# Kernel optimization log

Measured on AMD Instinct MI355X. Metric: run time of the kernel, lower is better.

Reference implementation:

```python
import jax, jax.numpy as jnp
import numpy as np

D_MODEL = 1024
NUM_HEADS = 16
D_FF = 4096
EPS = 1e-5


def _linear(x, w, b):
    # torch nn.Linear: y = x @ W^T + b, W is [out, in]
    return jnp.einsum('bld,od->blo', x, w) + b


def _layer_norm(x, g, b):
    mu = jnp.mean(x, axis=-1, keepdims=True)
    var = jnp.mean(jnp.square(x - mu), axis=-1, keepdims=True)
    return (x - mu) / jnp.sqrt(var + EPS) * g + b


def _mha(q, k, v, wq, bq, wk, bk, wv, bv, wo, bo, mask, num_heads):
    B, Lq, D = q.shape
    hd = D // num_heads
    Q = _linear(q, wq, bq).reshape(B, Lq, num_heads, hd).transpose(0, 2, 1, 3)
    K = _linear(k, wk, bk).reshape(B, -1, num_heads, hd).transpose(0, 2, 1, 3)
    V = _linear(v, wv, bv).reshape(B, -1, num_heads, hd).transpose(0, 2, 1, 3)
    scale = jnp.sqrt(jnp.asarray(hd, dtype=q.dtype))
    energy = jnp.einsum('bhqd,bhkd->bhqk', Q, K) / scale  # [B,H,Lq,Lk]
    energy = jnp.where(mask, energy, jnp.asarray(-1e10, dtype=q.dtype))
    attn = jax.nn.softmax(energy, axis=-1)
    x = jnp.einsum('bhqk,bhkd->bhqd', attn, V)
    x = x.transpose(0, 2, 1, 3).reshape(B, Lq, D)
    return _linear(x, wo, bo), attn


def setup_inputs() -> dict:
    key = jax.random.key(0)
    ks = iter(jax.random.split(key, 40))
    B, T, S, D, F = 4, 1024, 1024, D_MODEL, D_FF
    inp = {
        'tgt': jax.random.normal(next(ks), (B, T, D), dtype=jnp.float32),
        'enc_src': jax.random.normal(next(ks), (B, S, D), dtype=jnp.float32),
        'tgt_mask': jnp.tril(jnp.ones((1, 1, T, T), dtype=bool)),
        'src_mask': jnp.ones((1, 1, 1, S), dtype=bool),
    }
    def lin(kk, o, i):
        return jax.random.normal(kk, (o, i), dtype=jnp.float32) * 0.02
    for pfx in ('sa', 'ca'):  # self-attn and cross-attn params
        for nm in ('q', 'k', 'v', 'o'):
            inp[f'{pfx}_w{nm}'] = lin(next(ks), D, D)
            inp[f'{pfx}_b{nm}'] = jnp.zeros((D,), dtype=jnp.float32)
    inp['ff_w1'] = lin(next(ks), F, D)
    inp['ff_b1'] = jnp.zeros((F,), dtype=jnp.float32)
    inp['ff_w2'] = lin(next(ks), D, F)
    inp['ff_b2'] = jnp.zeros((D,), dtype=jnp.float32)
    for i in (1, 2, 3):
        inp[f'ln{i}_g'] = jnp.ones((D,), dtype=jnp.float32)
        inp[f'ln{i}_b'] = jnp.zeros((D,), dtype=jnp.float32)
    return inp


def reference(tgt, enc_src, tgt_mask, src_mask,
              sa_wq, sa_bq, sa_wk, sa_bk, sa_wv, sa_bv, sa_wo, sa_bo,
              ca_wq, ca_bq, ca_wk, ca_bk, ca_wv, ca_bv, ca_wo, ca_bo,
              ff_w1, ff_b1, ff_w2, ff_b2,
              ln1_g, ln1_b, ln2_g, ln2_b, ln3_g, ln3_b):
    # dropout in eval mode (identity)
    _t, _ = _mha(tgt, tgt, tgt, sa_wq, sa_bq, sa_wk, sa_bk, sa_wv, sa_bv,
                 sa_wo, sa_bo, tgt_mask, NUM_HEADS)
    tgt = _layer_norm(tgt + _t, ln1_g, ln1_b)
    _t, attention = _mha(tgt, enc_src, enc_src, ca_wq, ca_bq, ca_wk, ca_bk,
                         ca_wv, ca_bv, ca_wo, ca_bo, src_mask, NUM_HEADS)
    tgt = _layer_norm(tgt + _t, ln2_g, ln2_b)
    _t = _linear(jax.nn.relu(_linear(tgt, ff_w1, ff_b1)), ff_w2, ff_b2)
    tgt = _layer_norm(tgt + _t, ln3_g, ln3_b)
    return tgt, attention
```

## Files before the change

kernel.cpp:

```cpp
#include <hip/hip_runtime.h>
#include <hip/hip_bf16.h>

#define BBATCH 4
#define TT 1024
#define SS 1024
#define DD 1024
#define HH 16
#define HD 64
#define FFD 4096
#define MM (BBATCH*TT)

using f32x4  = __attribute__((ext_vector_type(4))) float;
using s16x8  = __attribute__((ext_vector_type(8))) short;
using bf16x8 = __attribute__((ext_vector_type(8))) __bf16;

__device__ __forceinline__ unsigned short f2b(float f) {
  union { float f; unsigned int u; } x{f};
  unsigned int r = x.u + 0x7FFFu + ((x.u >> 16) & 1u);
  return (unsigned short)(r >> 16);
}

__device__ __forceinline__ void gload16(const void* g, void* l) {
  __builtin_amdgcn_global_load_lds(
      (const __attribute__((address_space(1))) void*)g,
      (__attribute__((address_space(3))) void*)l, 16, 0, 0);
}

__device__ __forceinline__ f32x4 mfma_bf16(s16x8 a, s16x8 b, f32x4 c) {
  return __builtin_amdgcn_mfma_f32_16x16x32_bf16(
      __builtin_bit_cast(bf16x8, a), __builtin_bit_cast(bf16x8, b), c, 0, 0, 0);
}

template <int JT>
__device__ __forceinline__ void gemm_core(
    const unsigned short* __restrict__ Ab, int lda,
    const unsigned short* __restrict__ Bb, int ldb,
    int K, unsigned short* As, unsigned short* Bs, f32x4 (&acc)[4][JT])
{
  const int tid = threadIdx.x, wave = tid >> 6, lane = tid & 63;
  const int r0 = tid >> 2, c0 = (tid & 3) * 8;
  const int wrow = (wave >> 1) * 64, wcol = (wave & 1) * 16 * JT;
  const int q = lane >> 4, rl = lane & 15;
  const s16x8* Av = (const s16x8*)As;
  const s16x8* Bv = (const s16x8*)Bs;

  for (int k0 = 0; k0 < K; k0 += 32) {
    gload16(Ab + (size_t)r0 * lda + k0 + c0, As + wave * 512);
    gload16(Ab + (size_t)(r0 + 64) * lda + k0 + c0, As + wave * 512 + 2048);
    gload16(Bb + (size_t)r0 * ldb + k0 + c0, Bs + wave * 512);
    if (JT == 4)
      gload16(Bb + (size_t)(r0 + 64) * ldb + k0 + c0, Bs + wave * 512 + 2048);
    __syncthreads();
    s16x8 af[4], bfr[JT];
#pragma unroll
    for (int t = 0; t < 4; t++) af[t] = Av[(wrow + t * 16 + rl) * 4 + q];
#pragma unroll
    for (int t = 0; t < JT; t++) bfr[t] = Bv[(wcol + t * 16 + rl) * 4 + q];
#pragma unroll
    for (int i = 0; i < 4; i++)
#pragma unroll
      for (int j = 0; j < JT; j++)
        acc[i][j] = mfma_bf16(af[i], bfr[j], acc[i][j]);
    __syncthreads();
  }
}

template <int EPI, int JT>
__global__ __launch_bounds__(256) void gemm_bt(
    const unsigned short* __restrict__ A, int lda,
    const unsigned short* __restrict__ B, int ldb,
    const float* __restrict__ bias, const float* __restrict__ res,
    float* __restrict__ Cf, unsigned short* __restrict__ Cb, int ldc, int K)
{
  __shared__ __align__(16) unsigned short As[128 * 32];
  __shared__ __align__(16) unsigned short Bs[JT * 1024];
  const int bm = blockIdx.y, bn = blockIdx.x;
  const int lane = threadIdx.x & 63, wave = threadIdx.x >> 6;
  const int wrow = (wave >> 1) * 64, wcol = (wave & 1) * 16 * JT;
  const int q = lane >> 4, rl = lane & 15;

  f32x4 acc[4][JT];
  f32x4 z = {0.f, 0.f, 0.f, 0.f};
#pragma unroll
  for (int i = 0; i < 4; i++)
#pragma unroll
    for (int j = 0; j < JT; j++) acc[i][j] = z;

  gemm_core<JT>(A + (size_t)bm * 128 * lda, lda,
                B + (size_t)bn * (32 * JT) * ldb, ldb, K, As, Bs, acc);

#pragma unroll
  for (int i = 0; i < 4; i++) {
    int gm0 = bm * 128 + wrow + i * 16 + q * 4;
#pragma unroll
    for (int j = 0; j < JT; j++) {
      int gn = bn * (32 * JT) + wcol + j * 16 + rl;
      float bv = bias[gn];
#pragma unroll
      for (int r = 0; r < 4; r++) {
        size_t off = (size_t)(gm0 + r) * ldc + gn;
        float v = acc[i][j][r];
        if constexpr (EPI == 0) Cb[off] = f2b(v + bv);
        else if constexpr (EPI == 2) Cf[off] = v + bv + res[off];
        else Cb[off] = f2b(fmaxf(v + bv, 0.f));
      }
    }
  }
}

__device__ __forceinline__ void sblock_qk(
    const unsigned short* Qs, const unsigned short* Ks,
    int wrow, int wcol, int q, int rl, f32x4 (&acc)[4][4])
{
  const s16x8* Qv = (const s16x8*)Qs;
  const s16x8* Kv = (const s16x8*)Ks;
  f32x4 z = {0.f, 0.f, 0.f, 0.f};
#pragma unroll
  for (int i = 0; i < 4; i++)
#pragma unroll
    for (int j = 0; j < 4; j++) acc[i][j] = z;
#pragma unroll
  for (int kq = 0; kq < 2; kq++) {
    s16x8 af[4], bf[4];
#pragma unroll
    for (int t = 0; t < 4; t++) af[t] = Qv[kq * 512 + (wrow + t * 16 + rl) * 4 + q];
#pragma unroll
    for (int t = 0; t < 4; t++) bf[t] = Kv[kq * 512 + (wcol + t * 16 + rl) * 4 + q];
#pragma unroll
    for (int i = 0; i < 4; i++)
#pragma unroll
      for (int j = 0; j < 4; j++)
        acc[i][j] = mfma_bf16(af[i], bf[j], acc[i][j]);
  }
}

__global__ __launch_bounds__(256, 2) void flash_sa(
    const unsigned short* __restrict__ Qg, int ldq,
    const unsigned short* __restrict__ Kg, int ldk,
    const unsigned short* __restrict__ Vt,
    unsigned short* __restrict__ Og)
{
  __shared__ __align__(16) unsigned short Qs[2 * 128 * 32];
  __shared__ __align__(16) unsigned short KP[4 * 128 * 40];
  __shared__ __align__(16) unsigned short Vs[4 * 64 * 32];
  __shared__ float red[2][128];

  const int tid = threadIdx.x, wave = tid >> 6, lane = tid & 63;
  const int q = lane >> 4, rl = lane & 15;
  const int bm = blockIdx.x, bh = blockIdx.y, b = bh >> 4, h = bh & 15;
  const int wrow = (wave >> 1) * 64, wcol = (wave & 1) * 64;
  const int wc2 = (wave & 1) * 32;
  const int r0 = tid >> 2, c0 = (tid & 3) * 8;

  const unsigned short* Qbase = Qg + ((size_t)b * TT + bm * 128) * ldq + h * HD;
  const unsigned short* Kbase = Kg + (size_t)b * SS * ldk + h * HD;
  const unsigned short* Vbase = Vt + ((size_t)bh << 16);

#pragma unroll
  for (int kq = 0; kq < 2; kq++) {
    gload16(Qbase + (size_t)r0 * ldq + kq * 32 + c0, Qs + kq * 4096 + wave * 512);
    gload16(Qbase + (size_t)(r0 + 64) * ldq + kq * 32 + c0, Qs + kq * 4096 + wave * 512 + 2048);
  }
  const int nch = bm + 1;
  const float NEG = -3.0e38f;

  float m_run[4][4], l_run[4][4];
  f32x4 oacc[4][2];
  f32x4 z = {0.f, 0.f, 0.f, 0.f};
#pragma unroll
  for (int i = 0; i < 4; i++) {
    oacc[i][0] = z; oacc[i][1] = z;
#pragma unroll
    for (int r = 0; r < 4; r++) { m_run[i][r] = NEG; l_run[i][r] = 0.f; }
  }

  for (int c = 0; c < nch; c++) {
    const unsigned short* src = Kbase + (size_t)c * 128 * ldk;
#pragma unroll
    for (int kq = 0; kq < 2; kq++) {
      gload16(src + (size_t)r0 * ldk + kq * 32 + c0, KP + kq * 4096 + wave * 512);
      gload16(src + (size_t)(r0 + 64) * ldk + kq * 32 + c0, KP + kq * 4096 + wave * 512 + 2048);
    }
#pragma unroll
    for (int ks = 0; ks < 4; ks++)
      gload16(Vbase + (size_t)r0 * SS + c * 128 + ks * 32 + c0, Vs + ks * 2048 + wave * 512);
    __syncthreads();

    f32x4 acc[4][4];
    sblock_qk(Qs, KP, wrow, wcol, q, rl, acc);
#pragma unroll
    for (int i = 0; i < 4; i++)
#pragma unroll
      for (int j = 0; j < 4; j++)
#pragma unroll
        for (int r = 0; r < 4; r++) {
          float v = acc[i][j][r] * 0.125f;
          if (c == bm && (wcol + j * 16 + rl) > (wrow + i * 16 + q * 4 + r)) v = NEG;
          acc[i][j][r] = v;
        }
    float mx[4][4];
#pragma unroll
    for (int i = 0; i < 4; i++)
#pragma unroll
      for (int r = 0; r < 4; r++) {
        float m0 = fmaxf(fmaxf(acc[i][0][r], acc[i][1][r]), fmaxf(acc[i][2][r], acc[i][3][r]));
#pragma unroll
        for (int off = 1; off < 16; off <<= 1) m0 = fmaxf(m0, __shfl_xor(m0, off));
        mx[i][r] = m0;
      }
    if (rl == 0) {
#pragma unroll
      for (int i = 0; i < 4; i++)
#pragma unroll
        for (int r = 0; r < 4; r++)
          red[wave & 1][wrow + i * 16 + q * 4 + r] = mx[i][r];
    }
    __syncthreads();
    float mn[4][4];
#pragma unroll
    for (int i = 0; i < 4; i++)
#pragma unroll
      for (int r = 0; r < 4; r++) {
        int row = wrow + i * 16 + q * 4 + r;
        mn[i][r] = fmaxf(m_run[i][r], fmaxf(red[0][row], red[1][row]));
      }
    float cs[4][4];
#pragma unroll
    for (int i = 0; i < 4; i++)
#pragma unroll
      for (int r = 0; r < 4; r++) {
#pragma unroll
        for (int j = 0; j < 4; j++) acc[i][j][r] = __expf(acc[i][j][r] - mn[i][r]);
        float s = acc[i][0][r] + acc[i][1][r] + acc[i][2][r] + acc[i][3][r];
#pragma unroll
        for (int off = 1; off < 16; off <<= 1) s += __shfl_xor(s, off);
        cs[i][r] = s;
      }
    __syncthreads();
    if (rl == 0) {
#pragma unroll
      for (int i = 0; i < 4; i++)
#pragma unroll
        for (int r = 0; r < 4; r++)
          red[wave & 1][wrow + i * 16 + q * 4 + r] = cs[i][r];
    }
    __syncthreads();
#pragma unroll
    for (int i = 0; i < 4; i++)
#pragma unroll
      for (int r = 0; r < 4; r++) {
        int row = wrow + i * 16 + q * 4 + r;
        float tot = red[0][row] + red[1][row];
        float al = __expf(m_run[i][r] - mn[i][r]);
        l_run[i][r] = l_run[i][r] * al + tot;
        m_run[i][r] = mn[i][r];
        oacc[i][0][r] *= al;
        oacc[i][1][r] *= al;
      }
#pragma unroll
    for (int i = 0; i < 4; i++)
#pragma unroll
      for (int j = 0; j < 4; j++) {
        int col = wcol + j * 16 + rl;
        int ks = col >> 5, cc = col & 31;
#pragma unroll
        for (int r = 0; r < 4; r++)
          KP[ks * 5120 + (wrow + i * 16 + q * 4 + r) * 40 + cc] = f2b(acc[i][j][r]);
      }
    __syncthreads();
    const s16x8* Pv = (const s16x8*)KP;
    const s16x8* Vv = (const s16x8*)Vs;
#pragma unroll
    for (int ks = 0; ks < 4; ks++) {
      s16x8 af[4], bf[2];
#pragma unroll
      for (int t = 0; t < 4; t++) af[t] = Pv[ks * 640 + (wrow + t * 16 + rl) * 5 + q];
#pragma unroll
      for (int t = 0; t < 2; t++) bf[t] = Vv[ks * 256 + (wc2 + t * 16 + rl) * 4 + q];
#pragma unroll
      for (int i = 0; i < 4; i++)
#pragma unroll
        for (int jt = 0; jt < 2; jt++)
          oacc[i][jt] = mfma_bf16(af[i], bf[jt], oacc[i][jt]);
    }
    __syncthreads();
  }

  float invl[4][4];
#pragma unroll
  for (int i = 0; i < 4; i++)
#pragma unroll
    for (int r = 0; r < 4; r++) invl[i][r] = 1.0f / l_run[i][r];

#pragma unroll
  for (int i = 0; i < 4; i++)
#pragma unroll
    for (int jt = 0; jt < 2; jt++)
#pragma unroll
      for (int r = 0; r < 4; r++) {
        int row = bm * 128 + wrow + i * 16 + q * 4 + r;
        int col = h * HD + wc2 + jt * 16 + rl;
        Og[((size_t)b * TT + row) * DD + col] = f2b(oacc[i][jt][r] * invl[i][r]);
      }
}

template <bool CAUSAL, bool WRITE_P>
__global__ __launch_bounds__(256, 2) void flash_attn(
    const unsigned short* __restrict__ Qg, int ldq,
    const unsigned short* __restrict__ Kg, int ldk,
    const unsigned short* __restrict__ Vt,
    float* __restrict__ Pout,
    unsigned short* __restrict__ Og)
{
  __shared__ __align__(16) unsigned short Qs[2 * 128 * 32];
  __shared__ __align__(16) unsigned short KP[4 * 128 * 40];
  __shared__ __align__(16) unsigned short Vs[4 * 64 * 32];
  __shared__ float red[2][128];

  const int tid = threadIdx.x, wave = tid >> 6, lane = tid & 63;
  const int q = lane >> 4, rl = lane & 15;
  const int bm = blockIdx.x, bh = blockIdx.y, b = bh >> 4, h = bh & 15;
  const int wrow = (wave >> 1) * 64, wcol = (wave & 1) * 64;
  const int r0 = tid >> 2, c0 = (tid & 3) * 8;

  const unsigned short* Qbase = Qg + ((size_t)b * TT + bm * 128) * ldq + h * HD;
  const unsigned short* Kbase = Kg + (size_t)b * SS * ldk + h * HD;
  const unsigned short* Vbase = Vt + ((size_t)bh << 16);

#pragma unroll
  for (int kq = 0; kq < 2; kq++) {
    gload16(Qbase + (size_t)r0 * ldq + kq * 32 + c0, Qs + kq * 4096 + wave * 512);
    gload16(Qbase + (size_t)(r0 + 64) * ldq + kq * 32 + c0, Qs + kq * 4096 + wave * 512 + 2048);
  }
  const int nch = CAUSAL ? bm + 1 : 8;
  const float NEG = -3.0e38f;

  float m_run[4][4], l_run[4][4];
#pragma unroll
  for (int i = 0; i < 4; i++)
#pragma unroll
    for (int r = 0; r < 4; r++) { m_run[i][r] = NEG; l_run[i][r] = 0.f; }

  for (int c = 0; c < nch; c++) {
    const unsigned short* src = Kbase + (size_t)c * 128 * ldk;
#pragma unroll
    for (int kq = 0; kq < 2; kq++) {
      gload16(src + (size_t)r0 * ldk + kq * 32 + c0, KP + kq * 4096 + wave * 512);
      gload16(src + (size_t)(r0 + 64) * ldk + kq * 32 + c0, KP + kq * 4096 + wave * 512 + 2048);
    }
    __syncthreads();
    f32x4 acc[4][4];
    sblock_qk(Qs, KP, wrow, wcol, q, rl, acc);
#pragma unroll
    for (int i = 0; i < 4; i++)
#pragma unroll
      for (int j = 0; j < 4; j++)
#pragma unroll
        for (int r = 0; r < 4; r++) {
          float v = acc[i][j][r] * 0.125f;
          if (CAUSAL && c == bm && (wcol + j * 16 + rl) > (wrow + i * 16 + q * 4 + r)) v = NEG;
          acc[i][j][r] = v;
        }
    float mx[4][4];
#pragma unroll
    for (int i = 0; i < 4; i++)
#pragma unroll
      for (int r = 0; r < 4; r++) {
        float m0 = fmaxf(fmaxf(acc[i][0][r], acc[i][1][r]), fmaxf(acc[i][2][r], acc[i][3][r]));
#pragma unroll
        for (int off = 1; off < 16; off <<= 1) m0 = fmaxf(m0, __shfl_xor(m0, off));
        mx[i][r] = m0;
      }
    if (rl == 0) {
#pragma unroll
      for (int i = 0; i < 4; i++)
#pragma unroll
        for (int r = 0; r < 4; r++)
          red[wave & 1][wrow + i * 16 + q * 4 + r] = mx[i][r];
    }
    __syncthreads();
    float mn[4][4];
#pragma unroll
    for (int i = 0; i < 4; i++)
#pragma unroll
      for (int r = 0; r < 4; r++) {
        int row = wrow + i * 16 + q * 4 + r;
        mn[i][r] = fmaxf(m_run[i][r], fmaxf(red[0][row], red[1][row]));
      }
    float cs[4][4];
#pragma unroll
    for (int i = 0; i < 4; i++)
#pragma unroll
      for (int r = 0; r < 4; r++) {
        float s = __expf(acc[i][0][r] - mn[i][r]) + __expf(acc[i][1][r] - mn[i][r]) +
                  __expf(acc[i][2][r] - mn[i][r]) + __expf(acc[i][3][r] - mn[i][r]);
#pragma unroll
        for (int off = 1; off < 16; off <<= 1) s += __shfl_xor(s, off);
        cs[i][r] = s;
      }
    __syncthreads();
    if (rl == 0) {
#pragma unroll
      for (int i = 0; i < 4; i++)
#pragma unroll
        for (int r = 0; r < 4; r++)
          red[wave & 1][wrow + i * 16 + q * 4 + r] = cs[i][r];
    }
    __syncthreads();
#pragma unroll
    for (int i = 0; i < 4; i++)
#pragma unroll
      for (int r = 0; r < 4; r++) {
        int row = wrow + i * 16 + q * 4 + r;
        float tot = red[0][row] + red[1][row];
        l_run[i][r] = l_run[i][r] * __expf(m_run[i][r] - mn[i][r]) + tot;
        m_run[i][r] = mn[i][r];
      }
    __syncthreads();
  }

  float invl[4][4];
#pragma unroll
  for (int i = 0; i < 4; i++)
#pragma unroll
    for (int r = 0; r < 4; r++) invl[i][r] = 1.0f / l_run[i][r];

  const int wc2 = (wave & 1) * 32;
  f32x4 oacc[4][2];
  f32x4 z = {0.f, 0.f, 0.f, 0.f};
#pragma unroll
  for (int i = 0; i < 4; i++) { oacc[i][0] = z; oacc[i][1] = z; }

  for (int c = 0; c < nch; c++) {
    __syncthreads();
    const unsigned short* src = Kbase + (size_t)c * 128 * ldk;
#pragma unroll
    for (int kq = 0; kq < 2; kq++) {
      gload16(src + (size_t)r0 * ldk + kq * 32 + c0, KP + kq * 4096 + wave * 512);
      gload16(src + (size_t)(r0 + 64) * ldk + kq * 32 + c0, KP + kq * 4096 + wave * 512 + 2048);
    }
#pragma unroll
    for (int ks = 0; ks < 4; ks++)
      gload16(Vbase + (size_t)r0 * SS + c * 128 + ks * 32 + c0, Vs + ks * 2048 + wave * 512);
    __syncthreads();
    f32x4 acc[4][4];
    sblock_qk(Qs, KP, wrow, wcol, q, rl, acc);
#pragma unroll
    for (int i = 0; i < 4; i++)
#pragma unroll
      for (int j = 0; j < 4; j++)
#pragma unroll
        for (int r = 0; r < 4; r++) {
          float v = acc[i][j][r] * 0.125f;
          bool msk = CAUSAL && c == bm && (wcol + j * 16 + rl) > (wrow + i * 16 + q * 4 + r);
          acc[i][j][r] = msk ? 0.f : __expf(v - m_run[i][r]) * invl[i][r];
        }
    if (WRITE_P) {
      float* Pb = Pout + ((size_t)bh << 20) +
                  ((size_t)(bm * 128 + wrow + q * 4) << 10) + c * 128 + wcol + rl;
#pragma unroll
      for (int i = 0; i < 4; i++)
#pragma unroll
        for (int r = 0; r < 4; r++)
#pragma unroll
          for (int j = 0; j < 4; j++)
            Pb[(size_t)((i * 16 + r) << 10) + j * 16] = acc[i][j][r];
    }
    __syncthreads();
#pragma unroll
    for (int i = 0; i < 4; i++)
#pragma unroll
      for (int j = 0; j < 4; j++) {
        int col = wcol + j * 16 + rl;
        int ks = col >> 5, cc = col & 31;
#pragma unroll
        for (int r = 0; r < 4; r++)
          KP[ks * 5120 + (wrow + i * 16 + q * 4 + r) * 40 + cc] = f2b(acc[i][j][r]);
      }
    __syncthreads();
    const s16x8* Pv = (const s16x8*)KP;
    const s16x8* Vv = (const s16x8*)Vs;
#pragma unroll
    for (int ks = 0; ks < 4; ks++) {
      s16x8 af[4], bf[2];
#pragma unroll
      for (int t = 0; t < 4; t++) af[t] = Pv[ks * 640 + (wrow + t * 16 + rl) * 5 + q];
#pragma unroll
      for (int t = 0; t < 2; t++) bf[t] = Vv[ks * 256 + (wc2 + t * 16 + rl) * 4 + q];
#pragma unroll
      for (int i = 0; i < 4; i++)
#pragma unroll
        for (int jt = 0; jt < 2; jt++)
          oacc[i][jt] = mfma_bf16(af[i], bf[jt], oacc[i][jt]);
    }
  }

#pragma unroll
  for (int i = 0; i < 4; i++)
#pragma unroll
    for (int jt = 0; jt < 2; jt++)
#pragma unroll
      for (int r = 0; r < 4; r++) {
        int row = bm * 128 + wrow + i * 16 + q * 4 + r;
        int col = h * HD + wc2 + jt * 16 + rl;
        Og[((size_t)b * TT + row) * DD + col] = f2b(oacc[i][jt][r]);
      }
}

__global__ __launch_bounds__(256) void transpose_v(
    const unsigned short* __restrict__ V, int ldv, unsigned short* __restrict__ Vt)
{
  __shared__ unsigned short tile[64][68];
  const int bh = blockIdx.z, b = bh >> 4, h = bh & 15;
  const int s0 = blockIdx.x * 64;
  const int tid = threadIdx.x;
#pragma unroll
  for (int i = 0; i < 4; i++) {
    int idx = i * 256 + tid;
    int sl = idx >> 4, d0 = (idx & 15) * 4;
    ushort4 v = *(const ushort4*)&V[((size_t)b * SS + s0 + sl) * ldv + h * HD + d0];
    tile[sl][d0] = v.x; tile[sl][d0 + 1] = v.y; tile[sl][d0 + 2] = v.z; tile[sl][d0 + 3] = v.w;
  }
  __syncthreads();
#pragma unroll
  for (int i = 0; i < 4; i++) {
    int idx = i * 256 + tid;
    int d = idx >> 4, s4 = (idx & 15) * 4;
    ushort4 o = make_ushort4(tile[s4][d], tile[s4 + 1][d], tile[s4 + 2][d], tile[s4 + 3][d]);
    *(ushort4*)&Vt[((size_t)bh * HD + d) * SS + s0 + s4] = o;
  }
}

__global__ __launch_bounds__(256) void ln_k(
    const float* __restrict__ src, const float* __restrict__ g,
    const float* __restrict__ b, float* __restrict__ dstf,
    unsigned short* __restrict__ dstb)
{
  __shared__ float sh[10];
  const size_t row = blockIdx.x;
  const int tid = threadIdx.x;
  float4 v = ((const float4*)(src + (row << 10)))[tid];
  float s = v.x + v.y + v.z + v.w;
  float ss = v.x * v.x + v.y * v.y + v.z * v.z + v.w * v.w;
  for (int o = 32; o; o >>= 1) { s += __shfl_down(s, o); ss += __shfl_down(ss, o); }
  if ((tid & 63) == 0) { sh[tid >> 6] = s; sh[4 + (tid >> 6)] = ss; }
  __syncthreads();
  if (tid == 0) {
    sh[8] = sh[0] + sh[1] + sh[2] + sh[3];
    sh[9] = sh[4] + sh[5] + sh[6] + sh[7];
  }
  __syncthreads();
  const float mean = sh[8] * (1.0f / DD);
  const float var = sh[9] * (1.0f / DD) - mean * mean;
  const float inv = rsqrtf(var + 1e-5f);
  float4 gv = ((const float4*)g)[tid];
  float4 bv = ((const float4*)b)[tid];
  float4 y;
  y.x = (v.x - mean) * inv * gv.x + bv.x;
  y.y = (v.y - mean) * inv * gv.y + bv.y;
  y.z = (v.z - mean) * inv * gv.z + bv.z;
  y.w = (v.w - mean) * inv * gv.w + bv.w;
  if (dstf) ((float4*)(dstf + (row << 10)))[tid] = y;
  if (dstb) {
    ushort4 o = make_ushort4(f2b(y.x), f2b(y.y), f2b(y.z), f2b(y.w));
    ((ushort4*)(dstb + (row << 10)))[tid] = o;
  }
}

struct CvtArgs {
  const float* src[12];
  unsigned short* dst[12];
};

__global__ __launch_bounds__(256) void cvt_all(CvtArgs a) {
  constexpr int st[13] = {0,       1048576, 2097152, 2359296, 2621440,
                          2883584, 3145728, 3407872, 3670016, 3932160,
                          4194304, 5242880, 6291456};
  int i = blockIdx.x * 256 + threadIdx.x;
  int s = 0;
#pragma unroll
  for (int k = 1; k < 12; k++) s += (i >= st[k]) ? 1 : 0;
  int j = i - st[s];
  float4 v = ((const float4*)a.src[s])[j];
  ushort4 o = make_ushort4(f2b(v.x), f2b(v.y), f2b(v.z), f2b(v.w));
  ((ushort4*)a.dst[s])[j] = o;
}

__global__ __launch_bounds__(256) void bias_pack(
    const float* __restrict__ bq, const float* __restrict__ bk, const float* __restrict__ bv,
    const float* __restrict__ bk2, const float* __restrict__ bv2,
    float* __restrict__ bqkv, float* __restrict__ bkv)
{
  int i = blockIdx.x * 256 + threadIdx.x;
  if (i < 1024) bqkv[i] = bq[i];
  else if (i < 2048) bqkv[i] = bk[i - 1024];
  else if (i < 3072) bqkv[i] = bv[i - 2048];
  else if (i < 4096) bkv[i - 3072] = bk2[i - 3072];
  else if (i < 5120) bkv[i - 3072] = bv2[i - 4096 + 1024];
}


extern "C" void kernel_launch(void* const* d_in, const int* in_sizes, int n_in,
                              void* d_out, int out_size, void* d_ws, size_t ws_size,
                              hipStream_t stream)
{
  const float* tgt = (const float*)d_in[0];
  const float* enc = (const float*)d_in[1];
  const float* sa_wq = (const float*)d_in[4];  const float* sa_bq = (const float*)d_in[5];
  const float* sa_wk = (const float*)d_in[6];  const float* sa_bk = (const float*)d_in[7];
  const float* sa_wv = (const float*)d_in[8];  const float* sa_bv = (const float*)d_in[9];
  const float* sa_wo = (const float*)d_in[10]; const float* sa_bo = (const float*)d_in[11];
  const float* ca_wq = (const float*)d_in[12]; const float* ca_bq = (const float*)d_in[13];
  const float* ca_wk = (const float*)d_in[14]; const float* ca_bk = (const float*)d_in[15];
  const float* ca_wv = (const float*)d_in[16]; const float* ca_bv = (const float*)d_in[17];
  const float* ca_wo = (const float*)d_in[18]; const float* ca_bo = (const float*)d_in[19];
  const float* ff_w1 = (const float*)d_in[20]; const float* ff_b1 = (const float*)d_in[21];
  const float* ff_w2 = (const float*)d_in[22]; const float* ff_b2 = (const float*)d_in[23];
  const float* ln1_g = (const float*)d_in[24]; const float* ln1_b = (const float*)d_in[25];
  const float* ln2_g = (const float*)d_in[26]; const float* ln2_b = (const float*)d_in[27];
  const float* ln3_g = (const float*)d_in[28]; const float* ln3_b = (const float*)d_in[29];

  float* out_tgt = (float*)d_out;
  float* out_attn = (float*)d_out + (size_t)MM * DD;

  char* w = (char*)d_ws;
  size_t off = 0;
  auto alloc = [&](size_t bytes) { void* p = w + off; off += (bytes + 255) & ~(size_t)255; return p; };
  unsigned short* Xb   = (unsigned short*)alloc((size_t)MM * DD * 2);
  unsigned short* Eb   = (unsigned short*)alloc((size_t)MM * DD * 2);
  unsigned short* Wq1  = (unsigned short*)alloc((size_t)DD * DD * 2);
  unsigned short* Wk1  = (unsigned short*)alloc((size_t)DD * DD * 2);
  unsigned short* Wv1  = (unsigned short*)alloc((size_t)DD * DD * 2);
  unsigned short* Wo1  = (unsigned short*)alloc((size_t)DD * DD * 2);
  unsigned short* Wq2  = (unsigned short*)alloc((size_t)DD * DD * 2);
  unsigned short* Wk2  = (unsigned short*)alloc((size_t)DD * DD * 2);
  unsigned short* Wv2  = (unsigned short*)alloc((size_t)DD * DD * 2);
  unsigned short* Wo2  = (unsigned short*)alloc((size_t)DD * DD * 2);
  unsigned short* Wf1  = (unsigned short*)alloc((size_t)FFD * DD * 2);
  unsigned short* Wf2  = (unsigned short*)alloc((size_t)DD * FFD * 2);
  unsigned short* QKVb = (unsigned short*)alloc((size_t)MM * 3 * DD * 2);
  unsigned short* KVb  = (unsigned short*)alloc((size_t)MM * 2 * DD * 2);
  unsigned short* Qca  = (unsigned short*)alloc((size_t)MM * DD * 2);
  unsigned short* Vt   = (unsigned short*)alloc((size_t)MM * DD * 2);
  unsigned short* Ob   = (unsigned short*)alloc((size_t)MM * DD * 2);
  float*          res1 = (float*)alloc((size_t)MM * DD * 4);
  unsigned short* t1b  = (unsigned short*)alloc((size_t)MM * DD * 2);
  float*          res2 = (float*)alloc((size_t)MM * DD * 4);
  unsigned short* t2b  = (unsigned short*)alloc((size_t)MM * DD * 2);
  unsigned short* Fb   = (unsigned short*)alloc((size_t)MM * FFD * 2);
  float*          bqkv = (float*)alloc(3072 * 4);
  float*          bkv  = (float*)alloc(2048 * 4);

  CvtArgs ca;
  ca.src[0] = tgt;   ca.dst[0] = Xb;
  ca.src[1] = enc;   ca.dst[1] = Eb;
  ca.src[2] = sa_wq; ca.dst[2] = Wq1;
  ca.src[3] = sa_wk; ca.dst[3] = Wk1;
  ca.src[4] = sa_wv; ca.dst[4] = Wv1;
  ca.src[5] = sa_wo; ca.dst[5] = Wo1;
  ca.src[6] = ca_wq; ca.dst[6] = Wq2;
  ca.src[7] = ca_wk; ca.dst[7] = Wk2;
  ca.src[8] = ca_wv; ca.dst[8] = Wv2;
  ca.src[9] = ca_wo; ca.dst[9] = Wo2;
  ca.src[10] = ff_w1; ca.dst[10] = Wf1;
  ca.src[11] = ff_w2; ca.dst[11] = Wf2;

  bias_pack<<<20, 256, 0, stream>>>(sa_bq, sa_bk, sa_bv, ca_bk, ca_bv, bqkv, bkv);
  cvt_all<<<24576, 256, 0, stream>>>(ca);

  const dim3 gQKV(24, 32);
  const dim3 gKV(16, 32);
  const dim3 gN64(16, 32);
  const dim3 gFF1(32, 32);
  const dim3 gFl(8, 64);
  const dim3 gTr(SS / 64, 1, BBATCH * HH);

  gemm_bt<0, 4><<<gQKV, 256, 0, stream>>>(Xb, DD, Wq1, DD, bqkv, nullptr, nullptr, QKVb, 3 * DD, DD);
  transpose_v<<<gTr, 256, 0, stream>>>(QKVb + 2 * DD, 3 * DD, Vt);
  flash_sa<<<gFl, 256, 0, stream>>>(QKVb, 3 * DD, QKVb + DD, 3 * DD, Vt, Ob);
  gemm_bt<2, 2><<<gN64, 256, 0, stream>>>(Ob, DD, Wo1, DD, sa_bo, tgt, res1, nullptr, DD, DD);
  ln_k<<<MM, 256, 0, stream>>>(res1, ln1_g, ln1_b, res1, t1b);

  gemm_bt<0, 2><<<gN64, 256, 0, stream>>>(t1b, DD, Wq2, DD, ca_bq, nullptr, nullptr, Qca, DD, DD);
  gemm_bt<0, 4><<<gKV, 256, 0, stream>>>(Eb, DD, Wk2, DD, bkv, nullptr, nullptr, KVb, 2 * DD, DD);
  transpose_v<<<gTr, 256, 0, stream>>>(KVb + DD, 2 * DD, Vt);
  flash_attn<false, true><<<gFl, 256, 0, stream>>>(Qca, DD, KVb, 2 * DD, Vt, out_attn, Ob);
  gemm_bt<2, 2><<<gN64, 256, 0, stream>>>(Ob, DD, Wo2, DD, ca_bo, res1, res2, nullptr, DD, DD);
  ln_k<<<MM, 256, 0, stream>>>(res2, ln2_g, ln2_b, res2, t2b);

  gemm_bt<3, 4><<<gFF1, 256, 0, stream>>>(t2b, DD, Wf1, DD, ff_b1, nullptr, nullptr, Fb, FFD, DD);
  gemm_bt<2, 2><<<gN64, 256, 0, stream>>>(Fb, FFD, Wf2, FFD, ff_b2, res2, res1, nullptr, DD, FFD);
  ln_k<<<MM, 256, 0, stream>>>(res1, ln3_g, ln3_b, out_tgt, nullptr);
}
```

Baseline: 866.4 us.

## Load K/V fragments directly from global, swizzle LDS, trim syncs, widen N-tiles

The flash attention kernels now read K and V MFMA fragments straight from global memory into registers instead of staging them through LDS. Q and P use an XOR-swizzled unpadded LDS layout in place of padded rows. Separate max and sum reduction buffers let several __syncthreads calls be removed. The cross-attention kernel becomes a dedicated non-templated version, and the N=1024 GEMMs switch to 128-wide N tiles with half the grid. The trade-off is less LDS traffic and barrier cost against uncoalesced per-lane global loads for K and V and lower GEMM block counts.

```diff
diff --git a/kernel.cpp b/kernel.cpp
--- a/kernel.cpp
+++ b/kernel.cpp
@@ -108,12 +108,22 @@
   }
 }
 
-__device__ __forceinline__ void sblock_qk(
-    const unsigned short* Qs, const unsigned short* Ks,
-    int wrow, int wcol, int q, int rl, f32x4 (&acc)[4][4])
+__device__ __forceinline__ void load_kf(
+    const unsigned short* Kp, int ldk, int wcol, int q, int rl, s16x8 (&kf)[2][4])
+{
+#pragma unroll
+  for (int j = 0; j < 4; j++) {
+    const unsigned short* p = Kp + (size_t)(wcol + j * 16 + rl) * ldk + q * 8;
+    kf[0][j] = *(const s16x8*)p;
+    kf[1][j] = *(const s16x8*)(p + 32);
+  }
+}
+
+__device__ __forceinline__ void qk_swz(
+    const unsigned short* Qs, const s16x8 (&kf)[2][4],
+    int wrow, int q, int rl, f32x4 (&acc)[4][4])
 {
   const s16x8* Qv = (const s16x8*)Qs;
-  const s16x8* Kv = (const s16x8*)Ks;
   f32x4 z = {0.f, 0.f, 0.f, 0.f};
 #pragma unroll
   for (int i = 0; i < 4; i++)
@@ -121,16 +131,59 @@
     for (int j = 0; j < 4; j++) acc[i][j] = z;
 #pragma unroll
   for (int kq = 0; kq < 2; kq++) {
-    s16x8 af[4], bf[4];
-#pragma unroll
-    for (int t = 0; t < 4; t++) af[t] = Qv[kq * 512 + (wrow + t * 16 + rl) * 4 + q];
-#pragma unroll
-    for (int t = 0; t < 4; t++) bf[t] = Kv[kq * 512 + (wcol + t * 16 + rl) * 4 + q];
+    s16x8 af[4];
+#pragma unroll
+    for (int t = 0; t < 4; t++) {
+      int row = wrow + t * 16 + rl;
+      af[t] = Qv[kq * 512 + ((row * 4 + q) ^ ((row >> 1) & 3))];
+    }
 #pragma unroll
     for (int i = 0; i < 4; i++)
 #pragma unroll
       for (int j = 0; j < 4; j++)
-        acc[i][j] = mfma_bf16(af[i], bf[j], acc[i][j]);
+        acc[i][j] = mfma_bf16(af[i], kf[kq][j], acc[i][j]);
+  }
+}
+
+__device__ __forceinline__ void store_ps(
+    unsigned short* Ps, const f32x4 (&acc)[4][4],
+    int wrow, int wcol, int q, int rl)
+{
+#pragma unroll
+  for (int i = 0; i < 4; i++)
+#pragma unroll
+    for (int j = 0; j < 4; j++) {
+      int col = wcol + j * 16 + rl;
+      int ks = col >> 5, cc = col & 31;
+#pragma unroll
+      for (int r = 0; r < 4; r++) {
+        int row = wrow + i * 16 + q * 4 + r;
+        Ps[ks * 4096 + ((row * 32 + cc) ^ (((row >> 1) & 3) << 3))] = f2b(acc[i][j][r]);
+      }
+    }
+}
+
+__device__ __forceinline__ void pv_accum(
+    const unsigned short* Ps, const unsigned short* Vbase, int c,
+    int wrow, int wc2, int q, int rl, f32x4 (&oacc)[4][2])
+{
+  const s16x8* Pv = (const s16x8*)Ps;
+#pragma unroll
+  for (int ks = 0; ks < 4; ks++) {
+    s16x8 af[4], bf[2];
+#pragma unroll
+    for (int t = 0; t < 4; t++) {
+      int row = wrow + t * 16 + rl;
+      af[t] = Pv[ks * 512 + ((row * 4 + q) ^ ((row >> 1) & 3))];
+    }
+#pragma unroll
+    for (int t = 0; t < 2; t++)
+      bf[t] = *(const s16x8*)(Vbase + (size_t)(wc2 + t * 16 + rl) * SS + c * 128 + ks * 32 + q * 8);
+#pragma unroll
+    for (int i = 0; i < 4; i++)
+#pragma unroll
+      for (int jt = 0; jt < 2; jt++)
+        oacc[i][jt] = mfma_bf16(af[i], bf[jt], oacc[i][jt]);
   }
 }
 
@@ -141,16 +194,16 @@
     unsigned short* __restrict__ Og)
 {
   __shared__ __align__(16) unsigned short Qs[2 * 128 * 32];
-  __shared__ __align__(16) unsigned short KP[4 * 128 * 40];
-  __shared__ __align__(16) unsigned short Vs[4 * 64 * 32];
-  __shared__ float red[2][128];
+  __shared__ __align__(16) unsigned short Ps[4 * 128 * 32];
+  __shared__ float redm[2][128], reds[2][128];
 
   const int tid = threadIdx.x, wave = tid >> 6, lane = tid & 63;
   const int q = lane >> 4, rl = lane & 15;
   const int bm = blockIdx.x, bh = blockIdx.y, b = bh >> 4, h = bh & 15;
   const int wrow = (wave >> 1) * 64, wcol = (wave & 1) * 64;
   const int wc2 = (wave & 1) * 32;
-  const int r0 = tid >> 2, c0 = (tid & 3) * 8;
+  const int r0 = tid >> 2;
+  const int c0s = ((tid & 3) ^ ((r0 >> 1) & 3)) * 8;
 
   const unsigned short* Qbase = Qg + ((size_t)b * TT + bm * 128) * ldq + h * HD;
   const unsigned short* Kbase = Kg + (size_t)b * SS * ldk + h * HD;
@@ -158,8 +211,8 @@
 
 #pragma unroll
   for (int kq = 0; kq < 2; kq++) {
-    gload16(Qbase + (size_t)r0 * ldq + kq * 32 + c0, Qs + kq * 4096 + wave * 512);
-    gload16(Qbase + (size_t)(r0 + 64) * ldq + kq * 32 + c0, Qs + kq * 4096 + wave * 512 + 2048);
+    gload16(Qbase + (size_t)r0 * ldq + kq * 32 + c0s, Qs + kq * 4096 + wave * 512);
+    gload16(Qbase + (size_t)(r0 + 64) * ldq + kq * 32 + c0s, Qs + kq * 4096 + wave * 512 + 2048);
   }
   const int nch = bm + 1;
   const float NEG = -3.0e38f;
@@ -173,21 +226,14 @@
 #pragma unroll
     for (int r = 0; r < 4; r++) { m_run[i][r] = NEG; l_run[i][r] = 0.f; }
   }
+  __syncthreads();
 
   for (int c = 0; c < nch; c++) {
-    const unsigned short* src = Kbase + (size_t)c * 128 * ldk;
-#pragma unroll
-    for (int kq = 0; kq < 2; kq++) {
-      gload16(src + (size_t)r0 * ldk + kq * 32 + c0, KP + kq * 4096 + wave * 512);
-      gload16(src + (size_t)(r0 + 64) * ldk + kq * 32 + c0, KP + kq * 4096 + wave * 512 + 2048);
-    }
-#pragma unroll
-    for (int ks = 0; ks < 4; ks++)
-      gload16(Vbase + (size_t)r0 * SS + c * 128 + ks * 32 + c0, Vs + ks * 2048 + wave * 512);
-    __syncthreads();
-
+    const unsigned short* Kp = Kbase + (size_t)c * 128 * ldk;
+    s16x8 kf[2][4];
+    load_kf(Kp, ldk, wcol, q, rl, kf);
     f32x4 acc[4][4];
-    sblock_qk(Qs, KP, wrow, wcol, q, rl, acc);
+    qk_swz(Qs, kf, wrow, q, rl, acc);
 #pragma unroll
     for (int i = 0; i < 4; i++)
 #pragma unroll
@@ -213,22 +259,16 @@
       for (int i = 0; i < 4; i++)
 #pragma unroll
         for (int r = 0; r < 4; r++)
-          red[wave & 1][wrow + i * 16 + q * 4 + r] = mx[i][r];
-    }
-    __syncthreads();
-    float mn[4][4];
+          redm[wave & 1][wrow + i * 16 + q * 4 + r] = mx[i][r];
+    }
+    __syncthreads();
+    float mn[4][4], cs[4][4];
 #pragma unroll
     for (int i = 0; i < 4; i++)
 #pragma unroll
       for (int r = 0; r < 4; r++) {
         int row = wrow + i * 16 + q * 4 + r;
-        mn[i][r] = fmaxf(m_run[i][r], fmaxf(red[0][row], red[1][row]));
-      }
-    float cs[4][4];
-#pragma unroll
-    for (int i = 0; i < 4; i++)
-#pragma unroll
-      for (int r = 0; r < 4; r++) {
+        mn[i][r] = fmaxf(m_run[i][r], fmaxf(redm[0][row], redm[1][row]));
 #pragma unroll
         for (int j = 0; j < 4; j++) acc[i][j][r] = __expf(acc[i][j][r] - mn[i][r]);
         float s = acc[i][0][r] + acc[i][1][r] + acc[i][2][r] + acc[i][3][r];
@@ -236,13 +276,13 @@
         for (int off = 1; off < 16; off <<= 1) s += __shfl_xor(s, off);
         cs[i][r] = s;
       }
-    __syncthreads();
+    store_ps(Ps, acc, wrow, wcol, q, rl);
     if (rl == 0) {
 #pragma unroll
       for (int i = 0; i < 4; i++)
 #pragma unroll
         for (int r = 0; r < 4; r++)
-          red[wave & 1][wrow + i * 16 + q * 4 + r] = cs[i][r];
+          reds[wave & 1][wrow + i * 16 + q * 4 + r] = cs[i][r];
     }
     __syncthreads();
 #pragma unroll
@@ -250,62 +290,32 @@
 #pragma unroll
       for (int r = 0; r < 4; r++) {
         int row = wrow + i * 16 + q * 4 + r;
-        float tot = red[0][row] + red[1][row];
+        float tot = reds[0][row] + reds[1][row];
         float al = __expf(m_run[i][r] - mn[i][r]);
         l_run[i][r] = l_run[i][r] * al + tot;
         m_run[i][r] = mn[i][r];
         oacc[i][0][r] *= al;
         oacc[i][1][r] *= al;
       }
-#pragma unroll
-    for (int i = 0; i < 4; i++)
-#pragma unroll
-      for (int j = 0; j < 4; j++) {
-        int col = wcol + j * 16 + rl;
-        int ks = col >> 5, cc = col & 31;
-#pragma unroll
-        for (int r = 0; r < 4; r++)
-          KP[ks * 5120 + (wrow + i * 16 + q * 4 + r) * 40 + cc] = f2b(acc[i][j][r]);
-      }
-    __syncthreads();
-    const s16x8* Pv = (const s16x8*)KP;
-    const s16x8* Vv = (const s16x8*)Vs;
-#pragma unroll
-    for (int ks = 0; ks < 4; ks++) {
-      s16x8 af[4], bf[2];
-#pragma unroll
-      for (int t = 0; t < 4; t++) af[t] = Pv[ks * 640 + (wrow + t * 16 + rl) * 5 + q];
-#pragma unroll
-      for (int t = 0; t < 2; t++) bf[t] = Vv[ks * 256 + (wc2 + t * 16 + rl) * 4 + q];
-#pragma unroll
-      for (int i = 0; i < 4; i++)
-#pragma unroll
-        for (int jt = 0; jt < 2; jt++)
-          oacc[i][jt] = mfma_bf16(af[i], bf[jt], oacc[i][jt]);
-    }
-    __syncthreads();
-  }
-
-  float invl[4][4];
-#pragma unroll
-  for (int i = 0; i < 4; i++)
-#pragma unroll
-    for (int r = 0; r < 4; r++) invl[i][r] = 1.0f / l_run[i][r];
-
-#pragma unroll
-  for (int i = 0; i < 4; i++)
-#pragma unroll
-    for (int jt = 0; jt < 2; jt++)
-#pragma unroll
-      for (int r = 0; r < 4; r++) {
-        int row = bm * 128 + wrow + i * 16 + q * 4 + r;
+    pv_accum(Ps, Vbase, c, wrow, wc2, q, rl, oacc);
+  }
+
+#pragma unroll
+  for (int i = 0; i < 4; i++) {
+#pragma unroll
+    for (int r = 0; r < 4; r++) {
+      float inv = 1.0f / l_run[i][r];
+      int row = bm * 128 + wrow + i * 16 + q * 4 + r;
+#pragma unroll
+      for (int jt = 0; jt < 2; jt++) {
         int col = h * HD + wc2 + jt * 16 + rl;
-        Og[((size_t)b * TT + row) * DD + col] = f2b(oacc[i][jt][r] * invl[i][r]);
-      }
-}
-
-template <bool CAUSAL, bool WRITE_P>
-__global__ __launch_bounds__(256, 2) void flash_attn(
+        Og[((size_t)b * TT + row) * DD + col] = f2b(oacc[i][jt][r] * inv);
+      }
+    }
+  }
+}
+
+__global__ __launch_bounds__(256, 2) void flash_ca(
     const unsigned short* __restrict__ Qg, int ldq,
     const unsigned short* __restrict__ Kg, int ldk,
     const unsigned short* __restrict__ Vt,
@@ -313,15 +323,16 @@
     unsigned short* __restrict__ Og)
 {
   __shared__ __align__(16) unsigned short Qs[2 * 128 * 32];
-  __shared__ __align__(16) unsigned short KP[4 * 128 * 40];
-  __shared__ __align__(16) unsigned short Vs[4 * 64 * 32];
-  __shared__ float red[2][128];
+  __shared__ __align__(16) unsigned short Ps[4 * 128 * 32];
+  __shared__ float redm[2][128], reds[2][128];
 
   const int tid = threadIdx.x, wave = tid >> 6, lane = tid & 63;
   const int q = lane >> 4, rl = lane & 15;
   const int bm = blockIdx.x, bh = blockIdx.y, b = bh >> 4, h = bh & 15;
   const int wrow = (wave >> 1) * 64, wcol = (wave & 1) * 64;
-  const int r0 = tid >> 2, c0 = (tid & 3) * 8;
+  const int wc2 = (wave & 1) * 32;
+  const int r0 = tid >> 2;
+  const int c0s = ((tid & 3) ^ ((r0 >> 1) & 3)) * 8;
 
   const unsigned short* Qbase = Qg + ((size_t)b * TT + bm * 128) * ldq + h * HD;
   const unsigned short* Kbase = Kg + (size_t)b * SS * ldk + h * HD;
@@ -329,10 +340,9 @@
 
 #pragma unroll
   for (int kq = 0; kq < 2; kq++) {
-    gload16(Qbase + (size_t)r0 * ldq + kq * 32 + c0, Qs + kq * 4096 + wave * 512);
-    gload16(Qbase + (size_t)(r0 + 64) * ldq + kq * 32 + c0, Qs + kq * 4096 + wave * 512 + 2048);
-  }
-  const int nch = CAUSAL ? bm + 1 : 8;
+    gload16(Qbase + (size_t)r0 * ldq + kq * 32 + c0s, Qs + kq * 4096 + wave * 512);
+    gload16(Qbase + (size_t)(r0 + 64) * ldq + kq * 32 + c0s, Qs + kq * 4096 + wave * 512 + 2048);
+  }
   const float NEG = -3.0e38f;
 
   float m_run[4][4], l_run[4][4];
@@ -340,32 +350,20 @@
   for (int i = 0; i < 4; i++)
 #pragma unroll
     for (int r = 0; r < 4; r++) { m_run[i][r] = NEG; l_run[i][r] = 0.f; }
-
-  for (int c = 0; c < nch; c++) {
-    const unsigned short* src = Kbase + (size_t)c * 128 * ldk;
-#pragma unroll
-    for (int kq = 0; kq < 2; kq++) {
-      gload16(src + (size_t)r0 * ldk + kq * 32 + c0, KP + kq * 4096 + wave * 512);
-      gload16(src + (size_t)(r0 + 64) * ldk + kq * 32 + c0, KP + kq * 4096 + wave * 512 + 2048);
-    }
-    __syncthreads();
+  __syncthreads();
+
+  for (int c = 0; c < 8; c++) {
+    s16x8 kf[2][4];
+    load_kf(Kbase + (size_t)c * 128 * ldk, ldk, wcol, q, rl, kf);
     f32x4 acc[4][4];
-    sblock_qk(Qs, KP, wrow, wcol, q, rl, acc);
-#pragma unroll
-    for (int i = 0; i < 4; i++)
-#pragma unroll
-      for (int j = 0; j < 4; j++)
-#pragma unroll
-        for (int r = 0; r < 4; r++) {
-          float v = acc[i][j][r] * 0.125f;
-          if (CAUSAL && c == bm && (wcol + j * 16 + rl) > (wrow + i * 16 + q * 4 + r)) v = NEG;
-          acc[i][j][r] = v;
-        }
+    qk_swz(Qs, kf, wrow, q, rl, acc);
     float mx[4][4];
 #pragma unroll
     for (int i = 0; i < 4; i++)
 #pragma unroll
       for (int r = 0; r < 4; r++) {
+#pragma unroll
+        for (int j = 0; j < 4; j++) acc[i][j][r] *= 0.125f;
         float m0 = fmaxf(fmaxf(acc[i][0][r], acc[i][1][r]), fmaxf(acc[i][2][r], acc[i][3][r]));
 #pragma unroll
         for (int off = 1; off < 16; off <<= 1) m0 = fmaxf(m0, __shfl_xor(m0, off));
@@ -376,35 +374,28 @@
       for (int i = 0; i < 4; i++)
 #pragma unroll
         for (int r = 0; r < 4; r++)
-          red[wave & 1][wrow + i * 16 + q * 4 + r] = mx[i][r];
-    }
-    __syncthreads();
-    float mn[4][4];
+          redm[wave & 1][wrow + i * 16 + q * 4 + r] = mx[i][r];
+    }
+    __syncthreads();
+    float mn[4][4], cs[4][4];
 #pragma unroll
     for (int i = 0; i < 4; i++)
 #pragma unroll
       for (int r = 0; r < 4; r++) {
         int row = wrow + i * 16 + q * 4 + r;
-        mn[i][r] = fmaxf(m_run[i][r], fmaxf(red[0][row], red[1][row]));
-      }
-    float cs[4][4];
-#pragma unroll
-    for (int i = 0; i < 4; i++)
-#pragma unroll
-      for (int r = 0; r < 4; r++) {
+        mn[i][r] = fmaxf(m_run[i][r], fmaxf(redm[0][row], redm[1][row]));
         float s = __expf(acc[i][0][r] - mn[i][r]) + __expf(acc[i][1][r] - mn[i][r]) +
                   __expf(acc[i][2][r] - mn[i][r]) + __expf(acc[i][3][r] - mn[i][r]);
 #pragma unroll
         for (int off = 1; off < 16; off <<= 1) s += __shfl_xor(s, off);
         cs[i][r] = s;
       }
-    __syncthreads();
     if (rl == 0) {
 #pragma unroll
       for (int i = 0; i < 4; i++)
 #pragma unroll
         for (int r = 0; r < 4; r++)
-          red[wave & 1][wrow + i * 16 + q * 4 + r] = cs[i][r];
+          reds[wave & 1][wrow + i * 16 + q * 4 + r] = cs[i][r];
     }
     __syncthreads();
 #pragma unroll
@@ -412,11 +403,10 @@
 #pragma unroll
       for (int r = 0; r < 4; r++) {
         int row = wrow + i * 16 + q * 4 + r;
-        float tot = red[0][row] + red[1][row];
+        float tot = reds[0][row] + reds[1][row];
         l_run[i][r] = l_run[i][r] * __expf(m_run[i][r] - mn[i][r]) + tot;
         m_run[i][r] = mn[i][r];
       }
-    __syncthreads();
   }
 
   float invl[4][4];
@@ -425,74 +415,36 @@
 #pragma unroll
     for (int r = 0; r < 4; r++) invl[i][r] = 1.0f / l_run[i][r];
 
-  const int wc2 = (wave & 1) * 32;
   f32x4 oacc[4][2];
   f32x4 z = {0.f, 0.f, 0.f, 0.f};
 #pragma unroll
   for (int i = 0; i < 4; i++) { oacc[i][0] = z; oacc[i][1] = z; }
 
-  for (int c = 0; c < nch; c++) {
-    __syncthreads();
-    const unsigned short* src = Kbase + (size_t)c * 128 * ldk;
-#pragma unroll
-    for (int kq = 0; kq < 2; kq++) {
-      gload16(src + (size_t)r0 * ldk + kq * 32 + c0, KP + kq * 4096 + wave * 512);
-      gload16(src + (size_t)(r0 + 64) * ldk + kq * 32 + c0, KP + kq * 4096 + wave * 512 + 2048);
-    }
-#pragma unroll
-    for (int ks = 0; ks < 4; ks++)
-      gload16(Vbase + (size_t)r0 * SS + c * 128 + ks * 32 + c0, Vs + ks * 2048 + wave * 512);
-    __syncthreads();
+  for (int c = 0; c < 8; c++) {
+    s16x8 kf[2][4];
+    load_kf(Kbase + (size_t)c * 128 * ldk, ldk, wcol, q, rl, kf);
     f32x4 acc[4][4];
-    sblock_qk(Qs, KP, wrow, wcol, q, rl, acc);
+    qk_swz(Qs, kf, wrow, q, rl, acc);
 #pragma unroll
     for (int i = 0; i < 4; i++)
 #pragma unroll
       for (int j = 0; j < 4; j++)
 #pragma unroll
-        for (int r = 0; r < 4; r++) {
-          float v = acc[i][j][r] * 0.125f;
-          bool msk = CAUSAL && c == bm && (wcol + j * 16 + rl) > (wrow + i * 16 + q * 4 + r);
-          acc[i][j][r] = msk ? 0.f : __expf(v - m_run[i][r]) * invl[i][r];
-        }
-    if (WRITE_P) {
-      float* Pb = Pout + ((size_t)bh << 20) +
-                  ((size_t)(bm * 128 + wrow + q * 4) << 10) + c * 128 + wcol + rl;
-#pragma unroll
-      for (int i = 0; i < 4; i++)
-#pragma unroll
         for (int r = 0; r < 4; r++)
-#pragma unroll
-          for (int j = 0; j < 4; j++)
-            Pb[(size_t)((i * 16 + r) << 10) + j * 16] = acc[i][j][r];
-    }
-    __syncthreads();
-#pragma unroll
-    for (int i = 0; i < 4; i++)
-#pragma unroll
-      for (int j = 0; j < 4; j++) {
-        int col = wcol + j * 16 + rl;
-        int ks = col >> 5, cc = col & 31;
-#pragma unroll
-        for (int r = 0; r < 4; r++)
-          KP[ks * 5120 + (wrow + i * 16 + q * 4 + r) * 40 + cc] = f2b(acc[i][j][r]);
-      }
-    __syncthreads();
-    const s16x8* Pv = (const s16x8*)KP;
-    const s16x8* Vv = (const s16x8*)Vs;
-#pragma unroll
-    for (int ks = 0; ks < 4; ks++) {
-      s16x8 af[4], bf[2];
-#pragma unroll
-      for (int t = 0; t < 4; t++) af[t] = Pv[ks * 640 + (wrow + t * 16 + rl) * 5 + q];
-#pragma unroll
-      for (int t = 0; t < 2; t++) bf[t] = Vv[ks * 256 + (wc2 + t * 16 + rl) * 4 + q];
-#pragma unroll
-      for (int i = 0; i < 4; i++)
-#pragma unroll
-        for (int jt = 0; jt < 2; jt++)
-          oacc[i][jt] = mfma_bf16(af[i], bf[jt], oacc[i][jt]);
-    }
+          acc[i][j][r] = __expf(acc[i][j][r] * 0.125f - m_run[i][r]) * invl[i][r];
+    float* Pb = Pout + ((size_t)bh << 20) +
+                ((size_t)(bm * 128 + wrow + q * 4) << 10) + c * 128 + wcol + rl;
+#pragma unroll
+    for (int i = 0; i < 4; i++)
+#pragma unroll
+      for (int r = 0; r < 4; r++)
+#pragma unroll
+        for (int j = 0; j < 4; j++)
+          Pb[(size_t)((i * 16 + r) << 10) + j * 16] = acc[i][j][r];
+    __syncthreads();
+    store_ps(Ps, acc, wrow, wcol, q, rl);
+    __syncthreads();
+    pv_accum(Ps, Vbase, c, wrow, wc2, q, rl, oacc);
   }
 
 #pragma unroll
@@ -670,7 +622,7 @@
 
   const dim3 gQKV(24, 32);
   const dim3 gKV(16, 32);
-  const dim3 gN64(16, 32);
+  const dim3 gN128(8, 32);
   const dim3 gFF1(32, 32);
   const dim3 gFl(8, 64);
   const dim3 gTr(SS / 64, 1, BBATCH * HH);
@@ -678,17 +630,17 @@
   gemm_bt<0, 4><<<gQKV, 256, 0, stream>>>(Xb, DD, Wq1, DD, bqkv, nullptr, nullptr, QKVb, 3 * DD, DD);
   transpose_v<<<gTr, 256, 0, stream>>>(QKVb + 2 * DD, 3 * DD, Vt);
   flash_sa<<<gFl, 256, 0, stream>>>(QKVb, 3 * DD, QKVb + DD, 3 * DD, Vt, Ob);
-  gemm_bt<2, 2><<<gN64, 256, 0, stream>>>(Ob, DD, Wo1, DD, sa_bo, tgt, res1, nullptr, DD, DD);
+  gemm_bt<2, 4><<<gN128, 256, 0, stream>>>(Ob, DD, Wo1, DD, sa_bo, tgt, res1, nullptr, DD, DD);
   ln_k<<<MM, 256, 0, stream>>>(res1, ln1_g, ln1_b, res1, t1b);
 
-  gemm_bt<0, 2><<<gN64, 256, 0, stream>>>(t1b, DD, Wq2, DD, ca_bq, nullptr, nullptr, Qca, DD, DD);
+  gemm_bt<0, 4><<<gN128, 256, 0, stream>>>(t1b, DD, Wq2, DD, ca_bq, nullptr, nullptr, Qca, DD, DD);
   gemm_bt<0, 4><<<gKV, 256, 0, stream>>>(Eb, DD, Wk2, DD, bkv, nullptr, nullptr, KVb, 2 * DD, DD);
   transpose_v<<<gTr, 256, 0, stream>>>(KVb + DD, 2 * DD, Vt);
-  flash_attn<false, true><<<gFl, 256, 0, stream>>>(Qca, DD, KVb, 2 * DD, Vt, out_attn, Ob);
-  gemm_bt<2, 2><<<gN64, 256, 0, stream>>>(Ob, DD, Wo2, DD, ca_bo, res1, res2, nullptr, DD, DD);
+  flash_ca<<<gFl, 256, 0, stream>>>(Qca, DD, KVb, 2 * DD, Vt, out_attn, Ob);
+  gemm_bt<2, 4><<<gN128, 256, 0, stream>>>(Ob, DD, Wo2, DD, ca_bo, res1, res2, nullptr, DD, DD);
   ln_k<<<MM, 256, 0, stream>>>(res2, ln2_g, ln2_b, res2, t2b);
 
   gemm_bt<3, 4><<<gFF1, 256, 0, stream>>>(t2b, DD, Wf1, DD, ff_b1, nullptr, nullptr, Fb, FFD, DD);
-  gemm_bt<2, 2><<<gN64, 256, 0, stream>>>(Fb, FFD, Wf2, FFD, ff_b2, res2, res1, nullptr, DD, FFD);
+  gemm_bt<2, 4><<<gN128, 256, 0, stream>>>(Fb, FFD, Wf2, FFD, ff_b2, res2, res1, nullptr, DD, FFD);
   ln_k<<<MM, 256, 0, stream>>>(res1, ln3_g, ln3_b, out_tgt, nullptr);
 }
```

Result: slower. 925.6 us (+6.8%).
